# Kernel tuning notes

Measured on AMD Instinct MI355X. Metric: run time of the kernel, lower is better.

## Reference

```python
import jax, jax.numpy as jnp
import numpy as np

H, DK, DV, D = 16, 64, 64, 1024  # num_heads, dk, dv, model_dim (H*DV == D)
B, S = 4, 2048

def setup_inputs() -> dict:
    key = jax.random.key(0)
    ks = jax.random.split(key, 10)
    sc = 0.02
    x  = jax.random.normal(ks[0], (B, S, D), dtype=jnp.float32)
    Wq = jax.random.normal(ks[1], (H, D, DK), dtype=jnp.float32) * sc
    bq = jax.random.normal(ks[2], (H, DK), dtype=jnp.float32) * sc
    Wk = jax.random.normal(ks[3], (H, D, DK), dtype=jnp.float32) * sc
    bk = jax.random.normal(ks[4], (H, DK), dtype=jnp.float32) * sc
    Wv = jax.random.normal(ks[5], (H, D, DV), dtype=jnp.float32) * sc
    bv = jax.random.normal(ks[6], (H, DV), dtype=jnp.float32) * sc
    Wo = jax.random.normal(ks[7], (H * DV, D), dtype=jnp.float32) * sc
    bo = jax.random.normal(ks[8], (D,), dtype=jnp.float32) * sc
    return {"x": x, "Wq": Wq, "bq": bq, "Wk": Wk, "bk": bk,
            "Wv": Wv, "bv": bv, "Wo": Wo, "bo": bo}

def reference(x, Wq, bq, Wk, bk, Wv, bv, Wo, bo):
    # Batched per-head projections: [B,S,D] x [H,D,dk] -> [B,H,S,dk]
    Qx = jnp.einsum('bsd,hdk->bhsk', x, Wq) + bq[None, :, None, :]
    Kx = jnp.einsum('bsd,hdk->bhsk', x, Wk) + bk[None, :, None, :]
    Vx = jnp.einsum('bsd,hdv->bhsv', x, Wv) + bv[None, :, None, :]
    scores = jnp.einsum('bhsk,bhtk->bhst', Qx, Kx) / jnp.sqrt(jnp.float32(DK))
    attn = jax.nn.softmax(scores, axis=-1)
    out = jnp.einsum('bhst,bhtv->bhsv', attn, Vx)  # [B,H,S,dv]
    # concat heads (head order matches the torch cat order) -> [B,S,H*dv]
    cat = out.transpose(0, 2, 1, 3).reshape(B, S, H * DV)
    return cat @ Wo + bo
```

## Files before the change

### kernel.cpp

```cpp
#include <hip/hip_runtime.h>
#include <hip/hip_bf16.h>
#include <stdint.h>

typedef __bf16 bf16;
typedef __bf16 bf16x8 __attribute__((ext_vector_type(8)));
typedef __bf16 bf16x4 __attribute__((ext_vector_type(4)));
typedef float  f32x4  __attribute__((ext_vector_type(4)));
typedef float  f32x16 __attribute__((ext_vector_type(16)));

#define H_   16
#define D_   1024
#define B_   4
#define S_   2048
#define M_   (B_*S_)
#define REGION 8388608LL

#define QSCALE 0.18033688011112042f


__global__ void cast_x_kernel(const float* __restrict__ x, bf16* __restrict__ xb) {
    const int i = blockIdx.x * 256 + threadIdx.x;
    const float4* src = reinterpret_cast<const float4*>(x) + (size_t)i * 2;
    float4 a = src[0], b = src[1];
    bf16x8 o;
    o[0]=(bf16)a.x; o[1]=(bf16)a.y; o[2]=(bf16)a.z; o[3]=(bf16)a.w;
    o[4]=(bf16)b.x; o[5]=(bf16)b.y; o[6]=(bf16)b.z; o[7]=(bf16)b.w;
    *reinterpret_cast<bf16x8*>(xb + (size_t)i * 8) = o;
}

__global__ void prep_wqkv_kernel(const float* __restrict__ Wq, const float* __restrict__ Wk,
                                 const float* __restrict__ Wv, const float* __restrict__ bq,
                                 const float* __restrict__ bk, const float* __restrict__ bv,
                                 bf16* __restrict__ WqkvT, float* __restrict__ qkvb) {
    const int t = blockIdx.x * 256 + threadIdx.x;
    const int n = t >> 7, d0 = (t & 127) << 3;
    const int which = n >> 10, hh = (n >> 6) & 15, dk = n & 63;
    const float* W = (which == 0) ? Wq : (which == 1) ? Wk : Wv;
    const float* src = W + (size_t)hh * 65536 + (size_t)d0 * 64 + dk;
    bf16x8 o;
#pragma unroll
    for (int i = 0; i < 8; ++i) o[i] = (bf16)src[(size_t)i * 64];
    *reinterpret_cast<bf16x8*>(WqkvT + (size_t)n * D_ + d0) = o;
    if (d0 == 0) {
        const float* bb = (which == 0) ? bq : (which == 1) ? bk : bv;
        qkvb[n] = bb[n & 1023];
    }
}

__global__ void prep_wo_kernel(const float* __restrict__ Wo, bf16* __restrict__ WoT) {
    __shared__ float tile[64][65];
    const int k0 = blockIdx.x * 64, n0 = blockIdx.y * 64;
    const int t = threadIdx.x;
#pragma unroll
    for (int i = 0; i < 16; ++i) {
        int idx = t + i * 256, r = idx >> 6, c = idx & 63;
        tile[r][c] = Wo[(size_t)(k0 + r) * D_ + n0 + c];
    }
    __syncthreads();
#pragma unroll
    for (int i = 0; i < 16; ++i) {
        int idx = t + i * 256, n = idx >> 6, k = idx & 63;
        WoT[(size_t)(n0 + n) * D_ + k0 + k] = (bf16)tile[k][n];
    }
}

template <int MODE>
__global__ __launch_bounds__(256, 3)
void gemm_kernel(const bf16* __restrict__ A, const bf16* __restrict__ Bt,
                 const float* __restrict__ bias, void* __restrict__ Cout) {
    const int K = 1024;
    __shared__ __attribute__((aligned(16))) uint8_t ldsb[32768];
    const int t = threadIdx.x, w = t >> 6, ln = t & 63;
    const int g = ln >> 4, c = ln & 15;
    const int wm = w >> 1, wn = w & 1;
    const int bm = blockIdx.x, bn = blockIdx.y;

    const bf16* Ab = A  + (size_t)bm * 128 * K;
    const bf16* Bb = Bt + (size_t)bn * 128 * K;

    f32x4 zero = {0.f, 0.f, 0.f, 0.f};
    f32x4 acc[4][4];
#pragma unroll
    for (int mi = 0; mi < 4; ++mi)
#pragma unroll
        for (int ni = 0; ni < 4; ++ni) acc[mi][ni] = zero;

    const int srow = ln >> 3;
    const int scol = ((ln & 7) ^ srow) * 8;

    for (int kt = 0; kt < 16; ++kt) {
        const int k0 = kt * 64;
        __syncthreads();
#pragma unroll
        for (int i = 0; i < 4; ++i) {
            const int call = w * 4 + i;
            const int row = call * 8 + srow;
            const bf16* ga = Ab + (size_t)row * K + k0 + scol;
            const bf16* gb = Bb + (size_t)row * K + k0 + scol;
            __builtin_amdgcn_global_load_lds(
                (const __attribute__((address_space(1))) void*)ga,
                (__attribute__((address_space(3))) void*)(ldsb + call * 1024), 16, 0, 0);
            __builtin_amdgcn_global_load_lds(
                (const __attribute__((address_space(1))) void*)gb,
                (__attribute__((address_space(3))) void*)(ldsb + 16384 + call * 1024), 16, 0, 0);
        }
        __syncthreads();
#pragma unroll
        for (int kc = 0; kc < 2; ++kc) {
            bf16x8 af[4], bfr[4];
#pragma unroll
            for (int mi = 0; mi < 4; ++mi) {
                const int lrow = wm * 64 + mi * 16 + c;
                const int cb = (kc * 64 + g * 16) ^ ((lrow & 7) << 4);
                af[mi] = *reinterpret_cast<const bf16x8*>(ldsb + lrow * 128 + cb);
            }
#pragma unroll
            for (int ni = 0; ni < 4; ++ni) {
                const int lrow = wn * 64 + ni * 16 + c;
                const int cb = (kc * 64 + g * 16) ^ ((lrow & 7) << 4);
                bfr[ni] = *reinterpret_cast<const bf16x8*>(ldsb + 16384 + lrow * 128 + cb);
            }
#pragma unroll
            for (int mi = 0; mi < 4; ++mi)
#pragma unroll
                for (int ni = 0; ni < 4; ++ni)
                    acc[mi][ni] = __builtin_amdgcn_mfma_f32_16x16x32_bf16(
                        af[mi], bfr[ni], acc[mi][ni], 0, 0, 0);
        }
    }

#pragma unroll
    for (int mi = 0; mi < 4; ++mi) {
#pragma unroll
        for (int ni = 0; ni < 4; ++ni) {
            const int mrow = bm * 128 + wm * 64 + mi * 16 + g * 4;
            const int ncol = bn * 128 + wn * 64 + ni * 16 + c;
            const float bv_ = bias[ncol];
            if (MODE == 0) {
                const int which = ncol >> 10, hh = (ncol >> 6) & 15, dk = ncol & 63;
                const size_t bh64 = (size_t)((mrow >> 11) * 16 + hh);
                const int sI = mrow & 2047;
                if (which == 2) {
                    bf16x4 p4;
#pragma unroll
                    for (int j = 0; j < 4; ++j) p4[j] = (bf16)(acc[mi][ni][j] + bv_);
                    *reinterpret_cast<bf16x4*>((bf16*)Cout + 2 * REGION +
                                               (bh64 * 64 + dk) * S_ + sI) = p4;
                } else {
                    const float sc = (which == 0) ? QSCALE : 1.0f;
                    bf16* dst = (bf16*)Cout + (size_t)which * REGION +
                                (bh64 * S_ + sI) * 64 + dk;
#pragma unroll
                    for (int j = 0; j < 4; ++j)
                        dst[(size_t)j * 64] = (bf16)((acc[mi][ni][j] + bv_) * sc);
                }
            } else {
#pragma unroll
                for (int j = 0; j < 4; ++j)
                    ((float*)Cout)[(size_t)(mrow + j) * D_ + ncol] = acc[mi][ni][j] + bv_;
            }
        }
    }
}


__global__ __launch_bounds__(256, 2)
void attn_kernel(const bf16* __restrict__ Q, const bf16* __restrict__ K,
                 const bf16* __restrict__ Vt, bf16* __restrict__ cat) {
    __shared__ __attribute__((aligned(16))) bf16 KsA[2][64 * 64];
    __shared__ __attribute__((aligned(16))) bf16 VsA[2][64 * 64];
    __shared__ float red[4][64];
    const int t = threadIdx.x, w = t >> 6, lane = t & 63;
    const int l31 = lane & 31, h = lane >> 5;
    const int ko = (w >> 1) & 1;

    const int bid = blockIdx.x;
    const int nid = (bid & 7) * 64 + (bid >> 3);
    const int bh = nid >> 3, qb = nid & 7;
    const int q0 = qb * 256 + w * 64;

    const bf16* Qg = Q  + ((size_t)bh * S_ + q0) * 64;
    const bf16* Kg = K  + (size_t)bh * S_ * 64;
    const bf16* Vg = Vt + (size_t)bh * 64 * S_;

    bf16x8 qf[2][4];
#pragma unroll
    for (int qt = 0; qt < 2; ++qt)
#pragma unroll
        for (int dc = 0; dc < 4; ++dc)
            qf[qt][dc] = *reinterpret_cast<const bf16x8*>(
                Qg + (size_t)(qt * 32 + l31) * 64 + dc * 16 + h * 8);

    const int sr = lane >> 3, ss = lane & 7;
    const int swz = (ss ^ sr) * 8;

    auto STAGE_KV = [&](int buf, int kv0) {
#pragma unroll
        for (int cc = 0; cc < 2; ++cc) {
            const int row = w * 16 + cc * 8;
            const int rr = row + sr;
            const int rs = (rr & ~12) | ((rr & 4) << 1) | ((rr & 8) >> 1);
            __builtin_amdgcn_global_load_lds(
                (const __attribute__((address_space(1))) void*)
                    (Kg + (size_t)(kv0 + rs) * 64 + swz),
                (__attribute__((address_space(3))) void*)(&KsA[buf][row * 64]), 16, 0, 0);
            __builtin_amdgcn_global_load_lds(
                (const __attribute__((address_space(1))) void*)
                    (Vg + (size_t)(rr) * S_ + kv0 + swz),
                (__attribute__((address_space(3))) void*)(&VsA[buf][row * 64]), 16, 0, 0);
        }
    };

    f32x16 fz;
#pragma unroll
    for (int j = 0; j < 16; ++j) fz[j] = 0.f;

    f32x16 o[2][2];
    f32x16 lsv[2];
#pragma unroll
    for (int qt = 0; qt < 2; ++qt) {
#pragma unroll
        for (int j = 0; j < 16; ++j) { o[qt][0][j] = 0.f; o[qt][1][j] = 0.f; lsv[qt][j] = 0.f; }
    }

    STAGE_KV(0, 0);
    for (int it = 0; it < 32; ++it) {
        __syncthreads();
        if (it + 1 < 32) STAGE_KV((it + 1) & 1, (it + 1) * 64);
        const bf16* ks = KsA[it & 1];
        const bf16* vs = VsA[it & 1];
#pragma unroll
        for (int kb2 = 0; kb2 < 2; ++kb2) {
            const int kb = kb2 ^ ko;
            bf16x8 kf[4];
#pragma unroll
            for (int dc = 0; dc < 4; ++dc) {
                const int row = kb * 32 + l31;
                const int slot = (2 * dc + h) ^ (row & 7);
                kf[dc] = *reinterpret_cast<const bf16x8*>(ks + row * 64 + slot * 8);
            }
            __builtin_amdgcn_s_setprio(1);
            f32x16 s0 = __builtin_amdgcn_mfma_f32_32x32x16_bf16(kf[0], qf[0][0], fz, 0, 0, 0);
            f32x16 s1 = __builtin_amdgcn_mfma_f32_32x32x16_bf16(kf[0], qf[1][0], fz, 0, 0, 0);
#pragma unroll
            for (int dc = 1; dc < 4; ++dc) {
                s0 = __builtin_amdgcn_mfma_f32_32x32x16_bf16(kf[dc], qf[0][dc], s0, 0, 0, 0);
                s1 = __builtin_amdgcn_mfma_f32_32x32x16_bf16(kf[dc], qf[1][dc], s1, 0, 0, 0);
            }
            __builtin_amdgcn_s_setprio(0);
            f32x16 p0, p1;
#pragma unroll
            for (int j = 0; j < 16; ++j) p0[j] = __builtin_amdgcn_exp2f(s0[j]);
#pragma unroll
            for (int j = 0; j < 16; ++j) p1[j] = __builtin_amdgcn_exp2f(s1[j]);
            lsv[0] += p0;
            lsv[1] += p1;
            bf16x8 a00, a01, a10, a11;
#pragma unroll
            for (int e = 0; e < 8; ++e) {
                a00[e] = (bf16)p0[e]; a01[e] = (bf16)p0[8 + e];
                a10[e] = (bf16)p1[e]; a11[e] = (bf16)p1[8 + e];
            }
            __builtin_amdgcn_s_setprio(1);
#pragma unroll
            for (int t2 = 0; t2 < 2; ++t2) {
#pragma unroll
                for (int nb = 0; nb < 2; ++nb) {
                    const int row = l31 + 32 * nb;
                    const int slot = (4 * kb + 2 * t2 + h) ^ (row & 7);
                    bf16x8 vf = *reinterpret_cast<const bf16x8*>(vs + row * 64 + slot * 8);
                    o[0][nb] = __builtin_amdgcn_mfma_f32_32x32x16_bf16(
                        t2 ? a01 : a00, vf, o[0][nb], 0, 0, 0);
                    o[1][nb] = __builtin_amdgcn_mfma_f32_32x32x16_bf16(
                        t2 ? a11 : a10, vf, o[1][nb], 0, 0, 0);
                }
            }
            __builtin_amdgcn_s_setprio(0);
        }
    }

#pragma unroll
    for (int qt = 0; qt < 2; ++qt) {
        float s = 0.f;
#pragma unroll
        for (int j = 0; j < 16; ++j) s += lsv[qt][j];
        s += __shfl_xor(s, 32, 64);
        if (h == 0) red[w][qt * 32 + l31] = 1.0f / s;
    }
    const int b = bh >> 4, hh = bh & 15;
#pragma unroll
    for (int qt = 0; qt < 2; ++qt)
#pragma unroll
        for (int j = 0; j < 16; ++j) {
            const int q = qt * 32 + (j & 3) + 8 * (j >> 2) + 4 * h;
            const float rr = red[w][q];
            bf16* dst = cat + ((size_t)b * S_ + q0 + q) * D_ + hh * 64 + l31;
            dst[0]  = (bf16)(o[qt][0][j] * rr);
            dst[32] = (bf16)(o[qt][1][j] * rr);
        }
}

extern "C" void kernel_launch(void* const* d_in, const int* in_sizes, int n_in,
                              void* d_out, int out_size, void* d_ws, size_t ws_size,
                              hipStream_t stream) {
    const float* x  = (const float*)d_in[0];
    const float* Wq = (const float*)d_in[1];
    const float* bq = (const float*)d_in[2];
    const float* Wk = (const float*)d_in[3];
    const float* bk = (const float*)d_in[4];
    const float* Wv = (const float*)d_in[5];
    const float* bv = (const float*)d_in[6];
    const float* Wo = (const float*)d_in[7];
    const float* bo = (const float*)d_in[8];
    float* out = (float*)d_out;
    char* ws = (char*)d_ws;

    bf16*  xb    = (bf16*)(ws);
    bf16*  cat   = (bf16*)(ws + 16777216LL);
    bf16*  WqkvT = (bf16*)(ws + 33554432LL);
    bf16*  WoT   = (bf16*)(ws + 39845888LL);
    float* qkvb  = (float*)(ws + 41943040LL);
    bf16*  Qb    = (bf16*)(ws + 41955328LL);
    bf16*  Kb    = Qb + REGION;
    bf16*  Vtb   = Qb + 2 * REGION;

    hipLaunchKernelGGL(cast_x_kernel, dim3(4096), dim3(256), 0, stream, x, xb);
    hipLaunchKernelGGL(prep_wqkv_kernel, dim3(1536), dim3(256), 0, stream,
                       Wq, Wk, Wv, bq, bk, bv, WqkvT, qkvb);
    hipLaunchKernelGGL(prep_wo_kernel, dim3(16, 16), dim3(256), 0, stream, Wo, WoT);
    hipLaunchKernelGGL((gemm_kernel<0>), dim3(64, 24), dim3(256), 0, stream,
                       xb, WqkvT, qkvb, (void*)Qb);
    hipLaunchKernelGGL(attn_kernel, dim3(512), dim3(256), 0, stream, Qb, Kb, Vtb, cat);
    hipLaunchKernelGGL((gemm_kernel<1>), dim3(64, 8), dim3(256), 0, stream,
                       cat, WoT, bo, (void*)out);
}
```

Baseline: 191.2 us.

## Software-pipeline attention PV matmul with QK and deepen KV staging

Moves the K/V shared-memory ring from two buffers to four and prefetches two tiles ahead. The per-tile barrier is replaced by an explicit vmcnt wait plus s_barrier. Inside each tile, the PV MFMAs of the previous 32-key half run interleaved with the QK MFMAs of the next half, so the exp2 and bf16 conversion latency overlaps matrix work; a final epilogue drains the last half. The cost is doubled LDS use (64KB K/V per block), which may reduce how many blocks fit per CU. The code also drops the per-wave kb ordering swizzle and adds register pressure from the carried P fragments.

```diff
diff --git a/kernel.cpp b/kernel.cpp
--- a/kernel.cpp
+++ b/kernel.cpp
@@ -167,12 +167,11 @@
 __global__ __launch_bounds__(256, 2)
 void attn_kernel(const bf16* __restrict__ Q, const bf16* __restrict__ K,
                  const bf16* __restrict__ Vt, bf16* __restrict__ cat) {
-    __shared__ __attribute__((aligned(16))) bf16 KsA[2][64 * 64];
-    __shared__ __attribute__((aligned(16))) bf16 VsA[2][64 * 64];
+    __shared__ __attribute__((aligned(16))) bf16 KsA[4][64 * 64];
+    __shared__ __attribute__((aligned(16))) bf16 VsA[4][64 * 64];
     __shared__ float red[4][64];
     const int t = threadIdx.x, w = t >> 6, lane = t & 63;
     const int l31 = lane & 31, h = lane >> 5;
-    const int ko = (w >> 1) & 1;
 
     const int bid = blockIdx.x;
     const int nid = (bid & 7) * 64 + (bid >> 3);
@@ -223,19 +222,25 @@
         for (int j = 0; j < 16; ++j) { o[qt][0][j] = 0.f; o[qt][1][j] = 0.f; lsv[qt][j] = 0.f; }
     }
 
+    bf16x8 pa00 = {}, pa01 = {}, pa10 = {}, pa11 = {};
+
     STAGE_KV(0, 0);
+    STAGE_KV(1, 64);
     for (int it = 0; it < 32; ++it) {
-        __syncthreads();
-        if (it + 1 < 32) STAGE_KV((it + 1) & 1, (it + 1) * 64);
-        const bf16* ks = KsA[it & 1];
-        const bf16* vs = VsA[it & 1];
-#pragma unroll
-        for (int kb2 = 0; kb2 < 2; ++kb2) {
-            const int kb = kb2 ^ ko;
+        if (it < 31) asm volatile("s_waitcnt vmcnt(4)" ::: "memory");
+        else         asm volatile("s_waitcnt vmcnt(0)" ::: "memory");
+        __builtin_amdgcn_s_barrier();
+        __builtin_amdgcn_sched_barrier(0);
+        if (it + 2 < 32) STAGE_KV((it + 2) & 3, (it + 2) * 64);
+        const bf16* ks  = KsA[it & 3];
+        const bf16* vsC = VsA[it & 3];
+        const bf16* vsP = VsA[(it + 3) & 3];
+
+        {
             bf16x8 kf[4];
 #pragma unroll
             for (int dc = 0; dc < 4; ++dc) {
-                const int row = kb * 32 + l31;
+                const int row = l31;
                 const int slot = (2 * dc + h) ^ (row & 7);
                 kf[dc] = *reinterpret_cast<const bf16x8*>(ks + row * 64 + slot * 8);
             }
@@ -247,6 +252,21 @@
                 s0 = __builtin_amdgcn_mfma_f32_32x32x16_bf16(kf[dc], qf[0][dc], s0, 0, 0, 0);
                 s1 = __builtin_amdgcn_mfma_f32_32x32x16_bf16(kf[dc], qf[1][dc], s1, 0, 0, 0);
             }
+            if (it > 0) {
+#pragma unroll
+                for (int t2 = 0; t2 < 2; ++t2) {
+#pragma unroll
+                    for (int nb = 0; nb < 2; ++nb) {
+                        const int row = l31 + 32 * nb;
+                        const int slot = (4 + 2 * t2 + h) ^ (row & 7);
+                        bf16x8 vf = *reinterpret_cast<const bf16x8*>(vsP + row * 64 + slot * 8);
+                        o[0][nb] = __builtin_amdgcn_mfma_f32_32x32x16_bf16(
+                            t2 ? pa01 : pa00, vf, o[0][nb], 0, 0, 0);
+                        o[1][nb] = __builtin_amdgcn_mfma_f32_32x32x16_bf16(
+                            t2 ? pa11 : pa10, vf, o[1][nb], 0, 0, 0);
+                    }
+                }
+            }
             __builtin_amdgcn_s_setprio(0);
             f32x16 p0, p1;
 #pragma unroll
@@ -255,28 +275,75 @@
             for (int j = 0; j < 16; ++j) p1[j] = __builtin_amdgcn_exp2f(s1[j]);
             lsv[0] += p0;
             lsv[1] += p1;
-            bf16x8 a00, a01, a10, a11;
 #pragma unroll
             for (int e = 0; e < 8; ++e) {
-                a00[e] = (bf16)p0[e]; a01[e] = (bf16)p0[8 + e];
-                a10[e] = (bf16)p1[e]; a11[e] = (bf16)p1[8 + e];
+                pa00[e] = (bf16)p0[e]; pa01[e] = (bf16)p0[8 + e];
+                pa10[e] = (bf16)p1[e]; pa11[e] = (bf16)p1[8 + e];
+            }
+        }
+
+        {
+            bf16x8 kf[4];
+#pragma unroll
+            for (int dc = 0; dc < 4; ++dc) {
+                const int row = 32 + l31;
+                const int slot = (2 * dc + h) ^ (row & 7);
+                kf[dc] = *reinterpret_cast<const bf16x8*>(ks + row * 64 + slot * 8);
             }
             __builtin_amdgcn_s_setprio(1);
+            f32x16 s0 = __builtin_amdgcn_mfma_f32_32x32x16_bf16(kf[0], qf[0][0], fz, 0, 0, 0);
+            f32x16 s1 = __builtin_amdgcn_mfma_f32_32x32x16_bf16(kf[0], qf[1][0], fz, 0, 0, 0);
+#pragma unroll
+            for (int dc = 1; dc < 4; ++dc) {
+                s0 = __builtin_amdgcn_mfma_f32_32x32x16_bf16(kf[dc], qf[0][dc], s0, 0, 0, 0);
+                s1 = __builtin_amdgcn_mfma_f32_32x32x16_bf16(kf[dc], qf[1][dc], s1, 0, 0, 0);
+            }
 #pragma unroll
             for (int t2 = 0; t2 < 2; ++t2) {
 #pragma unroll
                 for (int nb = 0; nb < 2; ++nb) {
                     const int row = l31 + 32 * nb;
-                    const int slot = (4 * kb + 2 * t2 + h) ^ (row & 7);
-                    bf16x8 vf = *reinterpret_cast<const bf16x8*>(vs + row * 64 + slot * 8);
+                    const int slot = (2 * t2 + h) ^ (row & 7);
+                    bf16x8 vf = *reinterpret_cast<const bf16x8*>(vsC + row * 64 + slot * 8);
                     o[0][nb] = __builtin_amdgcn_mfma_f32_32x32x16_bf16(
-                        t2 ? a01 : a00, vf, o[0][nb], 0, 0, 0);
+                        t2 ? pa01 : pa00, vf, o[0][nb], 0, 0, 0);
                     o[1][nb] = __builtin_amdgcn_mfma_f32_32x32x16_bf16(
-                        t2 ? a11 : a10, vf, o[1][nb], 0, 0, 0);
+                        t2 ? pa11 : pa10, vf, o[1][nb], 0, 0, 0);
                 }
             }
             __builtin_amdgcn_s_setprio(0);
-        }
+            f32x16 p0, p1;
+#pragma unroll
+            for (int j = 0; j < 16; ++j) p0[j] = __builtin_amdgcn_exp2f(s0[j]);
+#pragma unroll
+            for (int j = 0; j < 16; ++j) p1[j] = __builtin_amdgcn_exp2f(s1[j]);
+            lsv[0] += p0;
+            lsv[1] += p1;
+#pragma unroll
+            for (int e = 0; e < 8; ++e) {
+                pa00[e] = (bf16)p0[e]; pa01[e] = (bf16)p0[8 + e];
+                pa10[e] = (bf16)p1[e]; pa11[e] = (bf16)p1[8 + e];
+            }
+        }
+    }
+
+    {
+        const bf16* vs = VsA[31 & 3];
+        __builtin_amdgcn_s_setprio(1);
+#pragma unroll
+        for (int t2 = 0; t2 < 2; ++t2) {
+#pragma unroll
+            for (int nb = 0; nb < 2; ++nb) {
+                const int row = l31 + 32 * nb;
+                const int slot = (4 + 2 * t2 + h) ^ (row & 7);
+                bf16x8 vf = *reinterpret_cast<const bf16x8*>(vs + row * 64 + slot * 8);
+                o[0][nb] = __builtin_amdgcn_mfma_f32_32x32x16_bf16(
+                    t2 ? pa01 : pa00, vf, o[0][nb], 0, 0, 0);
+                o[1][nb] = __builtin_amdgcn_mfma_f32_32x32x16_bf16(
+                    t2 ? pa11 : pa10, vf, o[1][nb], 0, 0, 0);
+            }
+        }
+        __builtin_amdgcn_s_setprio(0);
     }
 
 #pragma unroll
```

Measured after the change: 191.4 us. About the same (+0.1%).
